# Performance work log

Hardware: AMD Instinct MI355X
Metric: run time of the kernel (lower is better)

The kernel has to match this reference:

```python
import jax, jax.numpy as jnp
import numpy as np

GROUP = 8      # args.group_size
HEADS = 8      # CAN_Layer num_heads
HID = 512      # CAN hidden_dim
EPS = 1e-5     # BatchNorm eps
INF = 1e6


def setup_inputs() -> dict:
    key = jax.random.key(0)
    ks = jax.random.split(key, 32)
    B, Lp, Ld, Dp, Dd = 32, 2048, 512, 1280, 768
    W = lambda k, shape: jax.random.normal(k, shape, jnp.float32) * 0.02
    inp = {
        "prot_embed": jax.random.normal(ks[0], (B, Lp, Dp), jnp.float32),
        "drug_embed": jax.random.normal(ks[1], (B, Ld, Dd), jnp.float32),
        "prot_mask": jax.random.randint(ks[2], (B, Lp), 0, 2).astype(bool),
        "drug_mask": jax.random.randint(ks[3], (B, Ld), 0, 2).astype(bool),
        "w_preg": W(ks[4], (Dp, HID)), "b_preg": jnp.zeros((HID,), jnp.float32),
        "w_dreg": W(ks[5], (Dd, HID)), "b_dreg": jnp.zeros((HID,), jnp.float32),
        # CAN q/k/v projections (no bias)
        "wqp": W(ks[6], (HID, HID)), "wkp": W(ks[7], (HID, HID)), "wvp": W(ks[8], (HID, HID)),
        "wqd": W(ks[9], (HID, HID)), "wkd": W(ks[10], (HID, HID)), "wvd": W(ks[11], (HID, HID)),
        # MLP decoder (input_dim = 1024)
        "w1": W(ks[12], (1024, 1024)), "b1": jnp.zeros((1024,), jnp.float32),
        "g1": jnp.ones((1024,), jnp.float32), "be1": jnp.zeros((1024,), jnp.float32),
        "w2": W(ks[13], (1024, 512)), "b2": jnp.zeros((512,), jnp.float32),
        "g2": jnp.ones((512,), jnp.float32), "be2": jnp.zeros((512,), jnp.float32),
        "w3": W(ks[14], (512, 256)), "b3": jnp.zeros((256,), jnp.float32),
        "g3": jnp.ones((256,), jnp.float32), "be3": jnp.zeros((256,), jnp.float32),
        "wo": W(ks[15], (256, 1)), "bo": jnp.zeros((1,), jnp.float32),
    }
    return inp


def _group(x, m):
    B, L, D = x.shape
    g = L // GROUP
    xg = x.reshape(B, g, GROUP, D).mean(2)          # [B, g, D]
    mg = m.reshape(B, g, GROUP).any(2)              # [B, g]
    return xg, mg


def _alpha(logits, mrow, mcol):
    # logits: [B, L1, L2, H]; masked softmax over axis 2, then zero invalid rows
    pair = (mrow[:, :, None] & mcol[:, None, :])[..., None]
    logits = jnp.where(pair, logits, logits - INF)
    a = jax.nn.softmax(logits, axis=2)
    return jnp.where(mrow[:, :, None, None], a, jnp.zeros_like(a))


def _bn(x, g, b):
    # training-mode BatchNorm1d: batch stats, biased variance
    mu = x.mean(0)
    var = x.var(0)
    return g * (x - mu) * jax.lax.rsqrt(var + EPS) + b


def reference(prot_embed, drug_embed, prot_mask, drug_mask,
              w_preg, b_preg, w_dreg, b_dreg,
              wqp, wkp, wvp, wqd, wkd, wvd,
              w1, b1, g1, be1, w2, b2, g2, be2, w3, b3, g3, be3, wo, bo):
    prot = prot_embed @ w_preg + b_preg            # [B, Lp, 512]
    drug = drug_embed @ w_dreg + b_dreg            # [B, Ld, 512]
    pg, mp = _group(prot, prot_mask)               # [B, Gp, 512]
    dg, md = _group(drug, drug_mask)               # [B, Gd, 512]

    hd = HID // HEADS
    heads = lambda x, w: (x @ w).reshape(x.shape[0], x.shape[1], HEADS, hd)
    qp, kp, vp = heads(pg, wqp), heads(pg, wkp), heads(pg, wvp)
    qd, kd, vd = heads(dg, wqd), heads(dg, wkd), heads(dg, wvd)

    att = lambda q, k: jnp.einsum('blhd,bkhd->blkh', q, k)  # no sqrt(d) scaling (as in source)
    app = _alpha(att(qp, kp), mp, mp)
    apd = _alpha(att(qp, kd), mp, md)
    adp = _alpha(att(qd, kp), md, mp)
    add = _alpha(att(qd, kd), md, md)

    mix = lambda a, v: jnp.einsum('blkh,bkhd->blhd', a, v).reshape(a.shape[0], a.shape[1], HID)
    pe = (mix(app, vp) + mix(apd, vd)) * 0.5       # [B, Gp, 512]
    de = (mix(adp, vp) + mix(add, vd)) * 0.5       # [B, Gd, 512]

    # agg_mode == 'mean': masked mean over grouped tokens
    mpf = mp.astype(pe.dtype)
    mdf = md.astype(de.dtype)
    p_emb = (pe * mpf[..., None]).sum(1) / mpf.sum(1)[:, None]
    d_emb = (de * mdf[..., None]).sum(1) / mdf.sum(1)[:, None]
    x = jnp.concatenate([p_emb, d_emb], axis=1)    # [B, 1024]

    x = _bn(jax.nn.relu(x @ w1 + b1), g1, be1)
    x = _bn(jax.nn.relu(x @ w2 + b2), g2, be2)
    x = _bn(jax.nn.relu(x @ w3 + b3), g3, be3)
    return jax.nn.sigmoid(x @ wo + bo)             # [B, 1]
```

## Files before the change

### kernel.cpp

```cpp
#include <hip/hip_runtime.h>
#include <hip/hip_bf16.h>
#include <math.h>

#define BATCH 32
#define LP 2048
#define LDRUG 512
#define DP 1280
#define DD 768
#define GP 256
#define GD 64
#define HID 512
#define NH 8
#define HD 64
#define NKEY 320
#define PST 328

typedef unsigned short ushort_t;
typedef __attribute__((ext_vector_type(8))) __bf16 bf16x8;
typedef __attribute__((ext_vector_type(8))) _Float16 f16x8;
typedef __attribute__((ext_vector_type(4))) float f32x4;

__device__ __forceinline__ ushort_t f2bf(float f) {
    unsigned int u = __float_as_uint(f);
    u += 0x7fff + ((u >> 16) & 1);
    return (ushort_t)(u >> 16);
}

__global__ void group_mean_kernel(const float* __restrict__ in,
                                  ushort_t* __restrict__ out, int D4, int total4) {
    int o = blockIdx.x * blockDim.x + threadIdx.x;
    if (o >= total4) return;
    int d = o % D4;
    long row = o / D4;
    const float4* p = (const float4*)in + row * 8 * (long)D4 + d;
    float4 s = {0.f, 0.f, 0.f, 0.f};
#pragma unroll
    for (int j = 0; j < 8; ++j) {
        float4 v = p[(long)j * D4];
        s.x += v.x; s.y += v.y; s.z += v.z; s.w += v.w;
    }
    uint2 r;
    r.x = (unsigned)f2bf(s.x * 0.125f) | ((unsigned)f2bf(s.y * 0.125f) << 16);
    r.y = (unsigned)f2bf(s.z * 0.125f) | ((unsigned)f2bf(s.w * 0.125f) << 16);
    *(uint2*)(out + (size_t)o * 4) = r;
}

__global__ void group_mask_kernel(const int* __restrict__ m,
                                  int* __restrict__ out, int total) {
    int o = blockIdx.x * blockDim.x + threadIdx.x;
    if (o >= total) return;
    const int* p = m + (long)o * 8;
    int any = 0;
#pragma unroll
    for (int j = 0; j < 8; ++j) any |= p[j];
    out[o] = any ? 1 : 0;
}

struct TransJobs {
    const float* src[8];
    ushort_t* dst[8];
    int K[8], N[8], base[8];
};
__global__ __launch_bounds__(256) void transpose_cast8_kernel(TransJobs J) {
    __shared__ float tile[32][33];
    int tidx = blockIdx.x;
    int j = 0;
#pragma unroll
    for (int i = 1; i < 8; ++i) if (tidx >= J.base[i]) j = i;
    const float* W = J.src[j];
    ushort_t* Wt = J.dst[j];
    int K = J.K[j], N = J.N[j];
    int local = tidx - J.base[j];
    int kt = local % (K / 32), nt = local / (K / 32);
    int k0 = kt * 32, n0 = nt * 32;
    int tx = threadIdx.x & 31, ty = threadIdx.x >> 5;
#pragma unroll
    for (int i = 0; i < 32; i += 8)
        tile[ty + i][tx] = W[(size_t)(k0 + ty + i) * N + n0 + tx];
    __syncthreads();
#pragma unroll
    for (int i = 0; i < 32; i += 8)
        Wt[(size_t)(n0 + ty + i) * K + k0 + tx] = f2bf(tile[tx][ty + i]);
}

__global__ __launch_bounds__(256) void mfma_gemm_kernel(
        const ushort_t* __restrict__ A, const ushort_t* __restrict__ Bt,
        const float* __restrict__ bias, ushort_t* __restrict__ C,
        int M, int N, int K) {
    __shared__ ushort_t As[128 * 32];
    __shared__ ushort_t Bs[128 * 32];
    const int t = threadIdx.x;
    const int m0 = blockIdx.y * 128, n0 = blockIdx.x * 128;
    const int wavebase = (t >> 6) * 64;
    const int lane = t & 63;
    const int lrow = lane & 15, quad = lane >> 4;
    const int m_base = ((t >> 6) >> 1) * 64;
    const int n_base = ((t >> 6) & 1) * 64;
    f32x4 acc[4][4] = {};

    for (int k0 = 0; k0 < K; k0 += 32) {
#pragma unroll
        for (int it = 0; it < 2; ++it) {
            int c = it * 256 + t;
            int row = c >> 2, kc = (c & 3) * 8;
            __builtin_amdgcn_global_load_lds(
                (const __attribute__((address_space(1))) void*)(A + (size_t)(m0 + row) * K + k0 + kc),
                (__attribute__((address_space(3))) void*)(As + (size_t)(it * 256 + wavebase) * 8),
                16, 0, 0);
            __builtin_amdgcn_global_load_lds(
                (const __attribute__((address_space(1))) void*)(Bt + (size_t)(n0 + row) * K + k0 + kc),
                (__attribute__((address_space(3))) void*)(Bs + (size_t)(it * 256 + wavebase) * 8),
                16, 0, 0);
        }
        __syncthreads();
        bf16x8 af[4], bfr[4];
#pragma unroll
        for (int i = 0; i < 4; ++i)
            af[i] = *(const bf16x8*)(As + (m_base + i * 16 + lrow) * 32 + quad * 8);
#pragma unroll
        for (int j = 0; j < 4; ++j)
            bfr[j] = *(const bf16x8*)(Bs + (n_base + j * 16 + lrow) * 32 + quad * 8);
#pragma unroll
        for (int i = 0; i < 4; ++i)
#pragma unroll
            for (int j = 0; j < 4; ++j)
                acc[i][j] = __builtin_amdgcn_mfma_f32_16x16x32_bf16(af[i], bfr[j], acc[i][j], 0, 0, 0);
        __syncthreads();
    }
#pragma unroll
    for (int i = 0; i < 4; ++i) {
#pragma unroll
        for (int j = 0; j < 4; ++j) {
            int n = n0 + n_base + j * 16 + lrow;
            float bv = bias ? bias[n] : 0.f;
#pragma unroll
            for (int r = 0; r < 4; ++r) {
                int m = m0 + m_base + i * 16 + quad * 4 + r;
                C[(size_t)m * N + n] = f2bf(acc[i][j][r] + bv);
            }
        }
    }
}

template<int G, int KEYOFF>
__global__ __launch_bounds__(256) void qkv_gemm_kernel(
        const ushort_t* __restrict__ A, const ushort_t* __restrict__ Bt,
        _Float16* __restrict__ C, _Float16* __restrict__ VT) {
    const int K = 512, N = 1536;
    __shared__ ushort_t As[128 * 32];
    __shared__ ushort_t Bs[128 * 32];
    const int t = threadIdx.x;
    const int m0 = blockIdx.y * 128, n0 = blockIdx.x * 128;
    const int wavebase = (t >> 6) * 64;
    const int lane = t & 63;
    const int lrow = lane & 15, quad = lane >> 4;
    const int m_base = ((t >> 6) >> 1) * 64;
    const int n_base = ((t >> 6) & 1) * 64;
    f32x4 acc[4][4] = {};

    for (int k0 = 0; k0 < K; k0 += 32) {
#pragma unroll
        for (int it = 0; it < 2; ++it) {
            int c = it * 256 + t;
            int row = c >> 2, kc = (c & 3) * 8;
            __builtin_amdgcn_global_load_lds(
                (const __attribute__((address_space(1))) void*)(A + (size_t)(m0 + row) * K + k0 + kc),
                (__attribute__((address_space(3))) void*)(As + (size_t)(it * 256 + wavebase) * 8),
                16, 0, 0);
            __builtin_amdgcn_global_load_lds(
                (const __attribute__((address_space(1))) void*)(Bt + (size_t)(n0 + row) * K + k0 + kc),
                (__attribute__((address_space(3))) void*)(Bs + (size_t)(it * 256 + wavebase) * 8),
                16, 0, 0);
        }
        __syncthreads();
        bf16x8 af[4], bfr[4];
#pragma unroll
        for (int i = 0; i < 4; ++i)
            af[i] = *(const bf16x8*)(As + (m_base + i * 16 + lrow) * 32 + quad * 8);
#pragma unroll
        for (int j = 0; j < 4; ++j)
            bfr[j] = *(const bf16x8*)(Bs + (n_base + j * 16 + lrow) * 32 + quad * 8);
#pragma unroll
        for (int i = 0; i < 4; ++i)
#pragma unroll
            for (int j = 0; j < 4; ++j)
                acc[i][j] = __builtin_amdgcn_mfma_f32_16x16x32_bf16(af[i], bfr[j], acc[i][j], 0, 0, 0);
        __syncthreads();
    }
#pragma unroll
    for (int i = 0; i < 4; ++i) {
#pragma unroll
        for (int j = 0; j < 4; ++j) {
            int n = n0 + n_base + j * 16 + lrow;
            int hh = (n - 1024) >> 6;
            int dd = n & 63;
#pragma unroll
            for (int r = 0; r < 4; ++r) {
                int m = m0 + m_base + i * 16 + quad * 4 + r;
                _Float16 hv = (_Float16)acc[i][j][r];
                if (n < 1024) {
                    C[(size_t)m * N + n] = hv;
                } else {
                    int b = m / G, g = m % G;
                    VT[((size_t)(b * 8 + hh) * 64 + dd) * NKEY + KEYOFF + g] = hv;
                }
            }
        }
    }
}

__global__ __launch_bounds__(256) void fused_attn_kernel(
        const _Float16* __restrict__ qkvp, const _Float16* __restrict__ qkvd,
        const _Float16* __restrict__ VT,
        const int* __restrict__ mg, const int* __restrict__ md,
        float* __restrict__ x) {
    __shared__ _Float16 Ks[NKEY * 64];
    __shared__ _Float16 Vs[64 * NKEY];
    __shared__ _Float16 Ps[64 * PST];
    __shared__ int cm[NKEY];
    const int t = threadIdx.x;
    const int mtile = blockIdx.x, bh = blockIdx.y;
    const int b = bh >> 3, h = bh & 7;
    const int lane = t & 63, wid = t >> 6;
    const int lrow = lane & 15, quad = lane >> 4;

    if (t < GP) cm[t] = mg[b * GP + t];
    if (t < GD) cm[GP + t] = md[b * GD + t];

    for (int c = wid; c < 40; c += 4) {
        int row = c * 8 + (lane >> 3);
        int g16 = (lane & 7) ^ (row & 7);
        const _Float16* src = (row < GP)
            ? qkvp + ((size_t)(b * GP + row) * 1536 + 512 + h * HD) + g16 * 8
            : qkvd + ((size_t)(b * GD + row - GP) * 1536 + 512 + h * HD) + g16 * 8;
        __builtin_amdgcn_global_load_lds(
            (const __attribute__((address_space(1))) void*)src,
            (__attribute__((address_space(3))) void*)(Ks + (size_t)c * 512),
            16, 0, 0);
    }
    for (int c = wid; c < 40; c += 4) {
        int f = c * 64 + lane;
        int d = f / 40, c16 = f - d * 40;
        int gc = c16 ^ (d & 7);
        const _Float16* src = VT + ((size_t)bh * 64 + d) * NKEY + gc * 8;
        __builtin_amdgcn_global_load_lds(
            (const __attribute__((address_space(1))) void*)src,
            (__attribute__((address_space(3))) void*)(Vs + (size_t)c * 512),
            16, 0, 0);
    }

    const _Float16* Qb = (mtile < 4)
        ? qkvp + ((size_t)(b * GP + mtile * 64) * 1536 + h * HD)
        : qkvd + ((size_t)(b * GD) * 1536 + h * HD);
    const _Float16* qr = Qb + (size_t)(wid * 16 + lrow) * 1536 + quad * 8;
    f16x8 qf0 = *(const f16x8*)(qr);
    f16x8 qf1 = *(const f16x8*)(qr + 32);

    __syncthreads();

    f32x4 sacc[20] = {};
#pragma unroll
    for (int nt = 0; nt < 20; ++nt) {
        int key = nt * 16 + lrow;
        int x0 = (quad ^ (key & 7)) * 8;
        int x1 = ((4 + quad) ^ (key & 7)) * 8;
        f16x8 k0 = *(const f16x8*)(Ks + key * 64 + x0);
        f16x8 k1 = *(const f16x8*)(Ks + key * 64 + x1);
        sacc[nt] = __builtin_amdgcn_mfma_f32_16x16x32_f16(qf0, k0, sacc[nt], 0, 0, 0);
        sacc[nt] = __builtin_amdgcn_mfma_f32_16x16x32_f16(qf1, k1, sacc[nt], 0, 0, 0);
    }

    int cmk[20];
#pragma unroll
    for (int nt = 0; nt < 20; ++nt) cmk[nt] = cm[nt * 16 + lrow];
    const int rbase = mtile * 64 + wid * 16 + quad * 4;
#pragma unroll
    for (int r = 0; r < 4; ++r) {
        int mrow = cm[rbase + r];
        float xv[20];
#pragma unroll
        for (int nt = 0; nt < 20; ++nt)
            xv[nt] = sacc[nt][r] - (cmk[nt] ? 0.f : 1e6f);
        float mx = xv[0];
#pragma unroll
        for (int nt = 1; nt < 16; ++nt) mx = fmaxf(mx, xv[nt]);
#pragma unroll
        for (int off = 1; off < 16; off <<= 1) mx = fmaxf(mx, __shfl_xor(mx, off));
        float e[20];
        float s = 0.f;
#pragma unroll
        for (int nt = 0; nt < 16; ++nt) { e[nt] = __expf(xv[nt] - mx); s += e[nt]; }
#pragma unroll
        for (int off = 1; off < 16; off <<= 1) s += __shfl_xor(s, off);
        float sp = mrow ? (1.f / s) : 0.f;
        float mx2 = fmaxf(fmaxf(xv[16], xv[17]), fmaxf(xv[18], xv[19]));
#pragma unroll
        for (int off = 1; off < 16; off <<= 1) mx2 = fmaxf(mx2, __shfl_xor(mx2, off));
        float s2 = 0.f;
#pragma unroll
        for (int nt = 16; nt < 20; ++nt) { e[nt] = __expf(xv[nt] - mx2); s2 += e[nt]; }
#pragma unroll
        for (int off = 1; off < 16; off <<= 1) s2 += __shfl_xor(s2, off);
        float sp2 = mrow ? (1.f / s2) : 0.f;
        int m = wid * 16 + quad * 4 + r;
#pragma unroll
        for (int nt = 0; nt < 16; ++nt)
            Ps[m * PST + nt * 16 + lrow] = (_Float16)(e[nt] * sp);
#pragma unroll
        for (int nt = 16; nt < 20; ++nt)
            Ps[m * PST + nt * 16 + lrow] = (_Float16)(e[nt] * sp2);
    }
    __syncthreads();

    f32x4 oacc[4] = {};
#pragma unroll
    for (int kt = 0; kt < 10; ++kt) {
        f16x8 pa = *(const f16x8*)(Ps + (wid * 16 + lrow) * PST + kt * 32 + quad * 8);
#pragma unroll
        for (int nf = 0; nf < 4; ++nf) {
            int d = nf * 16 + lrow;
            int c16 = (kt * 4 + quad) ^ (d & 7);
            f16x8 vb = *(const f16x8*)(Vs + d * NKEY + c16 * 8);
            oacc[nf] = __builtin_amdgcn_mfma_f32_16x16x32_f16(pa, vb, oacc[nf], 0, 0, 0);
        }
    }

    const int xoff = (mtile < 4) ? 0 : 512;
#pragma unroll
    for (int nf = 0; nf < 4; ++nf) {
        float cs = oacc[nf][0] + oacc[nf][1] + oacc[nf][2] + oacc[nf][3];
        cs += __shfl_xor(cs, 16);
        cs += __shfl_xor(cs, 32);
        if (quad == 0)
            atomicAdd(x + (size_t)b * 1024 + xoff + h * HD + nf * 16 + lrow, 0.5f * cs);
    }
}

__global__ void zero_x_kernel(float* __restrict__ x) {
    x[blockIdx.x * 256 + threadIdx.x] = 0.f;
}

__global__ void pool_div_kernel(float* __restrict__ x,
                                const int* __restrict__ mg, const int* __restrict__ md) {
    const int b = blockIdx.x, t = threadIdx.x;
    __shared__ float inv[2];
    if (t == 0) { int s = 0; for (int i = 0; i < GP; ++i) s += mg[b * GP + i] ? 1 : 0; inv[0] = 1.f / (float)s; }
    else if (t == 1) { int s = 0; for (int i = 0; i < GD; ++i) s += md[b * GD + i] ? 1 : 0; inv[1] = 1.f / (float)s; }
    __syncthreads();
    x[(size_t)b * 1024 + t] *= inv[t >> 9];
}

template<int K, int N>
__global__ __launch_bounds__(256) void mlp_gemm_tiled(
        const float* __restrict__ X, const float* __restrict__ W,
        float* __restrict__ Y) {
    __shared__ float Xs[K];
    __shared__ float red[4][64];
    const int m = blockIdx.x, n0 = blockIdx.y * 64;
    const int t = threadIdx.x;
    const int nl = t & 63, ks = t >> 6;
    for (int i = t; i < K; i += 256) Xs[i] = X[(size_t)m * K + i];
    __syncthreads();
    const int KC = K / 4;
    const float* Wp = W + (size_t)(ks * KC) * N + n0 + nl;
    const float* Xp = Xs + ks * KC;
    float acc = 0.f;
#pragma unroll 8
    for (int i = 0; i < KC; ++i)
        acc = fmaf(Xp[i], Wp[(size_t)i * N], acc);
    red[ks][nl] = acc;
    __syncthreads();
    if (t < 64) {
        float s = red[0][t] + red[1][t] + red[2][t] + red[3][t];
        Y[(size_t)m * N + n0 + t] = s;
    }
}

template<int N>
__global__ __launch_bounds__(256) void bn_relu_kernel(
        const float* __restrict__ Ysum, const float* __restrict__ bias,
        const float* __restrict__ gamma, const float* __restrict__ beta,
        float* __restrict__ Out) {
    const int t = threadIdx.x;
    const int tc = t & 63, rg = t >> 6;
    const int c = blockIdx.x * 64 + tc;
    float bv = bias[c];
    float h[8], ps = 0.f, pq = 0.f;
#pragma unroll
    for (int r = 0; r < 8; ++r) {
        float v = fmaxf(Ysum[(size_t)(rg * 8 + r) * N + c] + bv, 0.f);
        h[r] = v; ps += v; pq += v * v;
    }
    __shared__ float red[2][4][64];
    red[0][rg][tc] = ps; red[1][rg][tc] = pq;
    __syncthreads();
    float mu  = (red[0][0][tc] + red[0][1][tc] + red[0][2][tc] + red[0][3][tc]) * (1.f / 32.f);
    float msq = (red[1][0][tc] + red[1][1][tc] + red[1][2][tc] + red[1][3][tc]) * (1.f / 32.f);
    float sc = gamma[c] * rsqrtf(msq - mu * mu + 1e-5f);
    float sh = beta[c] - mu * sc;
#pragma unroll
    for (int r = 0; r < 8; ++r)
        Out[(size_t)(rg * 8 + r) * N + c] = h[r] * sc + sh;
}

__global__ void final_kernel(const float* __restrict__ H, const float* __restrict__ wo,
                             const float* __restrict__ bo, float* __restrict__ out) {
    const int b = blockIdx.x, lane = threadIdx.x;
    float p = 0.f;
#pragma unroll
    for (int j = 0; j < 4; ++j) {
        int idx = lane + j * 64;
        p += H[b * 256 + idx] * wo[idx];
    }
#pragma unroll
    for (int off = 32; off >= 1; off >>= 1) p += __shfl_xor(p, off);
    if (lane == 0) out[b] = 1.f / (1.f + expf(-(p + bo[0])));
}

extern "C" void kernel_launch(void* const* d_in, const int* in_sizes, int n_in,
                              void* d_out, int out_size, void* d_ws, size_t ws_size,
                              hipStream_t stream) {
    const float* prot_embed = (const float*)d_in[0];
    const float* drug_embed = (const float*)d_in[1];
    const int* prot_mask = (const int*)d_in[2];
    const int* drug_mask = (const int*)d_in[3];
    const float* w_preg = (const float*)d_in[4];
    const float* b_preg = (const float*)d_in[5];
    const float* w_dreg = (const float*)d_in[6];
    const float* b_dreg = (const float*)d_in[7];
    const float* wqp = (const float*)d_in[8];
    const float* wkp = (const float*)d_in[9];
    const float* wvp = (const float*)d_in[10];
    const float* wqd = (const float*)d_in[11];
    const float* wkd = (const float*)d_in[12];
    const float* wvd = (const float*)d_in[13];
    const float* w1 = (const float*)d_in[14];  const float* b1 = (const float*)d_in[15];
    const float* g1 = (const float*)d_in[16];  const float* be1 = (const float*)d_in[17];
    const float* w2 = (const float*)d_in[18];  const float* b2 = (const float*)d_in[19];
    const float* g2 = (const float*)d_in[20];  const float* be2 = (const float*)d_in[21];
    const float* w3 = (const float*)d_in[22];  const float* b3 = (const float*)d_in[23];
    const float* g3 = (const float*)d_in[24];  const float* be3 = (const float*)d_in[25];
    const float* wo = (const float*)d_in[26];  const float* bo = (const float*)d_in[27];

    ushort_t* pgm = (ushort_t*)d_ws;
    ushort_t* dgm = pgm + 10485760;
    ushort_t* wpreg_t = dgm + 1572864;
    ushort_t* wdreg_t = wpreg_t + 655360;
    ushort_t* wqkvp_t = wdreg_t + 393216;
    ushort_t* wqkvd_t = wqkvp_t + 786432;
    ushort_t* pg = wqkvd_t + 786432;
    ushort_t* dg = pg + 4194304;
    _Float16* qkvp = (_Float16*)(dg + 1048576);
    _Float16* qkvd = qkvp + 12582912;
    _Float16* VT   = qkvd + 3145728;
    int* mg = (int*)(VT + 5242880);
    int* md = mg + 8192;
    float* x  = (float*)dgm;
    float* s1 = x + 32768;
    float* h1 = s1 + 32768;
    float* s2 = h1 + 32768;
    float* h2 = s2 + 16384;
    float* s3 = h2 + 16384;
    float* h3 = s3 + 8192;

    group_mean_kernel<<<(BATCH * GP * DP / 4) / 256, 256, 0, stream>>>(prot_embed, pgm, DP / 4, BATCH * GP * DP / 4);
    group_mean_kernel<<<(BATCH * GD * DD / 4) / 256, 256, 0, stream>>>(drug_embed, dgm, DD / 4, BATCH * GD * DD / 4);
    group_mask_kernel<<<(BATCH * GP) / 256, 256, 0, stream>>>(prot_mask, mg, BATCH * GP);
    group_mask_kernel<<<(BATCH * GD) / 256, 256, 0, stream>>>(drug_mask, md, BATCH * GD);

    TransJobs J;
    J.src[0] = w_preg; J.dst[0] = wpreg_t; J.K[0] = DP;  J.N[0] = HID;
    J.src[1] = w_dreg; J.dst[1] = wdreg_t; J.K[1] = DD;  J.N[1] = HID;
    J.src[2] = wqp; J.dst[2] = wqkvp_t;              J.K[2] = HID; J.N[2] = HID;
    J.src[3] = wkp; J.dst[3] = wqkvp_t + 512 * 512;  J.K[3] = HID; J.N[3] = HID;
    J.src[4] = wvp; J.dst[4] = wqkvp_t + 1024 * 512; J.K[4] = HID; J.N[4] = HID;
    J.src[5] = wqd; J.dst[5] = wqkvd_t;              J.K[5] = HID; J.N[5] = HID;
    J.src[6] = wkd; J.dst[6] = wqkvd_t + 512 * 512;  J.K[6] = HID; J.N[6] = HID;
    J.src[7] = wvd; J.dst[7] = wqkvd_t + 1024 * 512; J.K[7] = HID; J.N[7] = HID;
    {
        int base = 0;
        for (int i = 0; i < 8; ++i) { J.base[i] = base; base += (J.K[i] / 32) * (J.N[i] / 32); }
        transpose_cast8_kernel<<<base, 256, 0, stream>>>(J);
    }

    mfma_gemm_kernel<<<dim3(HID / 128, (BATCH * GP) / 128), 256, 0, stream>>>(
        pgm, wpreg_t, b_preg, pg, BATCH * GP, HID, DP);
    mfma_gemm_kernel<<<dim3(HID / 128, (BATCH * GD) / 128), 256, 0, stream>>>(
        dgm, wdreg_t, b_dreg, dg, BATCH * GD, HID, DD);
    zero_x_kernel<<<128, 256, 0, stream>>>(x);
    qkv_gemm_kernel<GP, 0><<<dim3(1536 / 128, (BATCH * GP) / 128), 256, 0, stream>>>(
        pg, wqkvp_t, qkvp, VT);
    qkv_gemm_kernel<GD, GP><<<dim3(1536 / 128, (BATCH * GD) / 128), 256, 0, stream>>>(
        dg, wqkvd_t, qkvd, VT);

    fused_attn_kernel<<<dim3(5, BATCH * NH), 256, 0, stream>>>(qkvp, qkvd, VT, mg, md, x);

    pool_div_kernel<<<BATCH, 1024, 0, stream>>>(x, mg, md);

    mlp_gemm_tiled<1024, 1024><<<dim3(BATCH, 1024 / 64), 256, 0, stream>>>(x, w1, s1);
    bn_relu_kernel<1024><<<1024 / 64, 256, 0, stream>>>(s1, b1, g1, be1, h1);
    mlp_gemm_tiled<1024, 512><<<dim3(BATCH, 512 / 64), 256, 0, stream>>>(h1, w2, s2);
    bn_relu_kernel<512><<<512 / 64, 256, 0, stream>>>(s2, b2, g2, be2, h2);
    mlp_gemm_tiled<512, 256><<<dim3(BATCH, 256 / 64), 256, 0, stream>>>(h2, w3, s3);
    bn_relu_kernel<256><<<256 / 64, 256, 0, stream>>>(s3, b3, g3, be3, h3);
    final_kernel<<<BATCH, 64, 0, stream>>>(h3, wo, bo, (float*)d_out);
}
```

Baseline: 751.9 us.

## Reuse K smem for P in attention, split MLP GEMMs over K with atomics

The attention kernel drops the separate V and P shared-memory buffers. It reuses the K buffer for the swizzled probability matrix and reads V fragments straight from global memory, which cuts LDS footprint and should raise occupancy at the cost of more global reads and an extra barrier. The MLP GEMVs are split four ways along K across a third grid dimension and combined with atomicAdd into scratch buffers that are now zeroed up front, giving more parallel blocks. The pooling mask count becomes a wave-level reduction instead of a serial loop.

```diff
diff --git a/kernel.cpp b/kernel.cpp
--- a/kernel.cpp
+++ b/kernel.cpp
@@ -13,7 +13,6 @@
 #define NH 8
 #define HD 64
 #define NKEY 320
-#define PST 328
 
 typedef unsigned short ushort_t;
 typedef __attribute__((ext_vector_type(8))) __bf16 bf16x8;
@@ -214,9 +213,7 @@
         const _Float16* __restrict__ VT,
         const int* __restrict__ mg, const int* __restrict__ md,
         float* __restrict__ x) {
-    __shared__ _Float16 Ks[NKEY * 64];
-    __shared__ _Float16 Vs[64 * NKEY];
-    __shared__ _Float16 Ps[64 * PST];
+    __shared__ _Float16 KP[20480];
     __shared__ int cm[NKEY];
     const int t = threadIdx.x;
     const int mtile = blockIdx.x, bh = blockIdx.y;
@@ -235,17 +232,7 @@
             : qkvd + ((size_t)(b * GD + row - GP) * 1536 + 512 + h * HD) + g16 * 8;
         __builtin_amdgcn_global_load_lds(
             (const __attribute__((address_space(1))) void*)src,
-            (__attribute__((address_space(3))) void*)(Ks + (size_t)c * 512),
-            16, 0, 0);
-    }
-    for (int c = wid; c < 40; c += 4) {
-        int f = c * 64 + lane;
-        int d = f / 40, c16 = f - d * 40;
-        int gc = c16 ^ (d & 7);
-        const _Float16* src = VT + ((size_t)bh * 64 + d) * NKEY + gc * 8;
-        __builtin_amdgcn_global_load_lds(
-            (const __attribute__((address_space(1))) void*)src,
-            (__attribute__((address_space(3))) void*)(Vs + (size_t)c * 512),
+            (__attribute__((address_space(3))) void*)(KP + (size_t)c * 512),
             16, 0, 0);
     }
 
@@ -264,11 +251,12 @@
         int key = nt * 16 + lrow;
         int x0 = (quad ^ (key & 7)) * 8;
         int x1 = ((4 + quad) ^ (key & 7)) * 8;
-        f16x8 k0 = *(const f16x8*)(Ks + key * 64 + x0);
-        f16x8 k1 = *(const f16x8*)(Ks + key * 64 + x1);
+        f16x8 k0 = *(const f16x8*)(KP + key * 64 + x0);
+        f16x8 k1 = *(const f16x8*)(KP + key * 64 + x1);
         sacc[nt] = __builtin_amdgcn_mfma_f32_16x16x32_f16(qf0, k0, sacc[nt], 0, 0, 0);
         sacc[nt] = __builtin_amdgcn_mfma_f32_16x16x32_f16(qf1, k1, sacc[nt], 0, 0, 0);
     }
+    __syncthreads();
 
     int cmk[20];
 #pragma unroll
@@ -304,23 +292,25 @@
         float sp2 = mrow ? (1.f / s2) : 0.f;
         int m = wid * 16 + quad * 4 + r;
 #pragma unroll
-        for (int nt = 0; nt < 16; ++nt)
-            Ps[m * PST + nt * 16 + lrow] = (_Float16)(e[nt] * sp);
-#pragma unroll
-        for (int nt = 16; nt < 20; ++nt)
-            Ps[m * PST + nt * 16 + lrow] = (_Float16)(e[nt] * sp2);
-    }
-    __syncthreads();
-
+        for (int nt = 0; nt < 20; ++nt) {
+            float pv = (nt < 16) ? e[nt] * sp : e[nt] * sp2;
+            int c16 = (nt * 2 + (lrow >> 3)) ^ (m & 7);
+            KP[m * 320 + c16 * 8 + (lrow & 7)] = (_Float16)pv;
+        }
+    }
+    __syncthreads();
+
+    const _Float16* Vb = VT + (size_t)bh * HD * NKEY;
     f32x4 oacc[4] = {};
 #pragma unroll
     for (int kt = 0; kt < 10; ++kt) {
-        f16x8 pa = *(const f16x8*)(Ps + (wid * 16 + lrow) * PST + kt * 32 + quad * 8);
+        int q = wid * 16 + lrow;
+        int c16 = (kt * 4 + quad) ^ (q & 7);
+        f16x8 pa = *(const f16x8*)(KP + q * 320 + c16 * 8);
 #pragma unroll
         for (int nf = 0; nf < 4; ++nf) {
             int d = nf * 16 + lrow;
-            int c16 = (kt * 4 + quad) ^ (d & 7);
-            f16x8 vb = *(const f16x8*)(Vs + d * NKEY + c16 * 8);
+            f16x8 vb = *(const f16x8*)(Vb + (size_t)d * NKEY + kt * 32 + quad * 8);
             oacc[nf] = __builtin_amdgcn_mfma_f32_16x16x32_f16(pa, vb, oacc[nf], 0, 0, 0);
         }
     }
@@ -336,16 +326,27 @@
     }
 }
 
-__global__ void zero_x_kernel(float* __restrict__ x) {
-    x[blockIdx.x * 256 + threadIdx.x] = 0.f;
+__global__ void zero_scratch_kernel(float* __restrict__ p) {
+    p[blockIdx.x * 256 + threadIdx.x] = 0.f;
 }
 
 __global__ void pool_div_kernel(float* __restrict__ x,
                                 const int* __restrict__ mg, const int* __restrict__ md) {
     const int b = blockIdx.x, t = threadIdx.x;
     __shared__ float inv[2];
-    if (t == 0) { int s = 0; for (int i = 0; i < GP; ++i) s += mg[b * GP + i] ? 1 : 0; inv[0] = 1.f / (float)s; }
-    else if (t == 1) { int s = 0; for (int i = 0; i < GD; ++i) s += md[b * GD + i] ? 1 : 0; inv[1] = 1.f / (float)s; }
+    if (t < 64) {
+        int s = 0;
+        for (int i = t; i < GP; i += 64) s += mg[b * GP + i] ? 1 : 0;
+#pragma unroll
+        for (int off = 32; off >= 1; off >>= 1) s += __shfl_xor(s, off);
+        if (t == 0) inv[0] = 1.f / (float)s;
+    } else if (t < 128) {
+        int l = t - 64;
+        int s = md[b * GD + l] ? 1 : 0;
+#pragma unroll
+        for (int off = 32; off >= 1; off >>= 1) s += __shfl_xor(s, off);
+        if (l == 0) inv[1] = 1.f / (float)s;
+    }
     __syncthreads();
     x[(size_t)b * 1024 + t] *= inv[t >> 9];
 }
@@ -354,15 +355,17 @@
 __global__ __launch_bounds__(256) void mlp_gemm_tiled(
         const float* __restrict__ X, const float* __restrict__ W,
         float* __restrict__ Y) {
-    __shared__ float Xs[K];
+    const int KB = K / 4;
+    __shared__ float Xs[KB];
     __shared__ float red[4][64];
-    const int m = blockIdx.x, n0 = blockIdx.y * 64;
+    const int m = blockIdx.x, n0 = blockIdx.y * 64, kb = blockIdx.z;
     const int t = threadIdx.x;
     const int nl = t & 63, ks = t >> 6;
-    for (int i = t; i < K; i += 256) Xs[i] = X[(size_t)m * K + i];
-    __syncthreads();
-    const int KC = K / 4;
-    const float* Wp = W + (size_t)(ks * KC) * N + n0 + nl;
+    const float* Xg = X + (size_t)m * K + (size_t)kb * KB;
+    for (int i = t; i < KB; i += 256) Xs[i] = Xg[i];
+    __syncthreads();
+    const int KC = KB / 4;
+    const float* Wp = W + (size_t)(kb * KB + ks * KC) * N + n0 + nl;
     const float* Xp = Xs + ks * KC;
     float acc = 0.f;
 #pragma unroll 8
@@ -372,7 +375,7 @@
     __syncthreads();
     if (t < 64) {
         float s = red[0][t] + red[1][t] + red[2][t] + red[3][t];
-        Y[(size_t)m * N + n0 + t] = s;
+        atomicAdd(Y + (size_t)m * N + n0 + t, s);
     }
 }
 
@@ -487,7 +490,7 @@
         pgm, wpreg_t, b_preg, pg, BATCH * GP, HID, DP);
     mfma_gemm_kernel<<<dim3(HID / 128, (BATCH * GD) / 128), 256, 0, stream>>>(
         dgm, wdreg_t, b_dreg, dg, BATCH * GD, HID, DD);
-    zero_x_kernel<<<128, 256, 0, stream>>>(x);
+    zero_scratch_kernel<<<576, 256, 0, stream>>>(x);
     qkv_gemm_kernel<GP, 0><<<dim3(1536 / 128, (BATCH * GP) / 128), 256, 0, stream>>>(
         pg, wqkvp_t, qkvp, VT);
     qkv_gemm_kernel<GD, GP><<<dim3(1536 / 128, (BATCH * GD) / 128), 256, 0, stream>>>(
@@ -497,11 +500,11 @@
 
     pool_div_kernel<<<BATCH, 1024, 0, stream>>>(x, mg, md);
 
-    mlp_gemm_tiled<1024, 1024><<<dim3(BATCH, 1024 / 64), 256, 0, stream>>>(x, w1, s1);
+    mlp_gemm_tiled<1024, 1024><<<dim3(BATCH, 1024 / 64, 4), 256, 0, stream>>>(x, w1, s1);
     bn_relu_kernel<1024><<<1024 / 64, 256, 0, stream>>>(s1, b1, g1, be1, h1);
-    mlp_gemm_tiled<1024, 512><<<dim3(BATCH, 512 / 64), 256, 0, stream>>>(h1, w2, s2);
+    mlp_gemm_tiled<1024, 512><<<dim3(BATCH, 512 / 64, 4), 256, 0, stream>>>(h1, w2, s2);
     bn_relu_kernel<512><<<512 / 64, 256, 0, stream>>>(s2, b2, g2, be2, h2);
-    mlp_gemm_tiled<512, 256><<<dim3(BATCH, 256 / 64), 256, 0, stream>>>(h2, w3, s3);
+    mlp_gemm_tiled<512, 256><<<dim3(BATCH, 256 / 64, 4), 256, 0, stream>>>(h2, w3, s3);
     bn_relu_kernel<256><<<256 / 64, 256, 0, stream>>>(s3, b3, g3, be3, h3);
     final_kernel<<<BATCH, 64, 0, stream>>>(h3, wo, bo, (float*)d_out);
 }
```

Result: faster. 721.4 us (-4.1%).
